# Kernel tuning notes

Measured on AMD Instinct MI355X. Metric: run time of the kernel, lower is better.

The kernel has to match this reference:

```python
import jax, jax.numpy as jnp
import numpy as np

N = 50000
E = 800000
DIM = 256
H = 8
D = DIM // H


def setup_inputs() -> dict:
    key = jax.random.key(0)
    ks = jax.random.split(key, 12)
    s = 1.0 / np.sqrt(DIM)
    return {
        "x": jax.random.normal(ks[0], (N, DIM), dtype=jnp.float32),
        "Wq": jax.random.normal(ks[1], (DIM, DIM), dtype=jnp.float32) * s,
        "bq": jax.random.normal(ks[2], (DIM,), dtype=jnp.float32) * 0.01,
        "Wk": jax.random.normal(ks[3], (DIM, DIM), dtype=jnp.float32) * s,
        "bk": jax.random.normal(ks[4], (DIM,), dtype=jnp.float32) * 0.01,
        "Wv": jax.random.normal(ks[5], (DIM, DIM), dtype=jnp.float32) * s,
        "bv": jax.random.normal(ks[6], (DIM,), dtype=jnp.float32) * 0.01,
        "Wo": jax.random.normal(ks[7], (DIM, DIM), dtype=jnp.float32) * s,
        "bo": jax.random.normal(ks[8], (DIM,), dtype=jnp.float32) * 0.01,
        "src": jax.random.randint(ks[9], (E,), 0, N, dtype=jnp.int32),
        "dst": jax.random.randint(ks[10], (E,), 0, N, dtype=jnp.int32),
    }


def reference(x, Wq, bq, Wk, bk, Wv, bv, Wo, bo, src, dst):
    # Linear projections (torch Linear: x @ W.T + b), then [N, H, D]
    q = (x @ Wq.T + bq).reshape(N, H, D)
    k = (x @ Wk.T + bk).reshape(N, H, D)
    v = (x @ Wv.T + bv).reshape(N, H, D)

    # u_dot_v: per-edge dot(queries[src], keys[dst]) -> [E, H]
    scores = jnp.einsum('ehd,ehd->eh', q[src], k[dst]) / jnp.sqrt(jnp.float32(D))

    # edge_softmax over incoming edges of each destination node
    smax = jax.ops.segment_max(scores, dst, num_segments=N)  # [N, H]
    e = jnp.exp(scores - smax[dst])                          # [E, H]
    ssum = jax.ops.segment_sum(e, dst, num_segments=N)       # [N, H]
    probs = e / ssum[dst]                                    # [E, H]

    # u_mul_e_sum: sum over incoming edges of values[src] * probs -> [N, H, D]
    out = jax.ops.segment_sum(v[src] * probs[:, :, None], dst, num_segments=N)

    out = out.reshape(N, DIM)
    return out @ Wo.T + bo  # dropout is identity at p=0 / eval
```

## Files before the change

### kernel.cpp

```cpp
#include <hip/hip_runtime.h>
#include <hip/hip_bf16.h>
#include <math.h>

#define DIMV 256
#define DV 32
#define QKVS 768

typedef __attribute__((ext_vector_type(8))) short bf16x8;
typedef __attribute__((ext_vector_type(4))) float f32x4;

#define EXPS(x) __expf(x)
#define SCORE_SCALE 0.17677669529663687f

static __device__ __forceinline__ unsigned short f2bf(float f) {
    unsigned x = __float_as_uint(f);
    x += 0x7FFF + ((x >> 16) & 1);
    return (unsigned short)(x >> 16);
}
static __device__ __forceinline__ float bf2f(unsigned short u) {
    return __uint_as_float(((unsigned)u) << 16);
}

static __device__ __forceinline__ void async16(const void* g, void* lds) {
    __builtin_amdgcn_global_load_lds(
        (const __attribute__((address_space(1))) void*)g,
        (__attribute__((address_space(3))) void*)lds, 16, 0, 0);
}


__global__ void cvt_w_count(const float* __restrict__ Wq, const float* __restrict__ Wk,
                            const float* __restrict__ Wv, const float* __restrict__ Wo,
                            unsigned short* __restrict__ Wcat,
                            const int* __restrict__ dst, int* __restrict__ deg, int E) {
    const float* W = blockIdx.y == 0 ? Wq : blockIdx.y == 1 ? Wk : blockIdx.y == 2 ? Wv : Wo;
    int i = blockIdx.x * 256 + threadIdx.x;
    float4 v = ((const float4*)W)[i];
    ushort4 o;
    o.x = f2bf(v.x); o.y = f2bf(v.y); o.z = f2bf(v.z); o.w = f2bf(v.w);
    ((ushort4*)(Wcat + (size_t)blockIdx.y * 65536))[i] = o;

    int gid = (blockIdx.y * gridDim.x + blockIdx.x) * 256 + threadIdx.x;
    int nthr = gridDim.x * gridDim.y * 256;
    for (int e = gid; e < E; e += nthr) atomicAdd(&deg[dst[e]], 1);
}


__global__ void zero_i32(int* __restrict__ p, int n) {
    int i = blockIdx.x * blockDim.x + threadIdx.x;
    if (i < n) p[i] = 0;
}

__global__ void block_sum(const int* __restrict__ deg, int* __restrict__ bsum, int n) {
    __shared__ int sm[256];
    int i = blockIdx.x * 256 + threadIdx.x;
    sm[threadIdx.x] = (i < n) ? deg[i] : 0;
    __syncthreads();
    for (int s = 128; s > 0; s >>= 1) {
        if (threadIdx.x < s) sm[threadIdx.x] += sm[threadIdx.x + s];
        __syncthreads();
    }
    if (threadIdx.x == 0) bsum[blockIdx.x] = sm[0];
}

__global__ void scan_bsum(int* __restrict__ bsum, int nb) {
    if (threadIdx.x == 0) {
        int r = 0;
        for (int i = 0; i < nb; ++i) { int v = bsum[i]; bsum[i] = r; r += v; }
    }
}

__global__ void scan_final(const int* __restrict__ deg, const int* __restrict__ bsum,
                           int* __restrict__ offsets, int* __restrict__ cursor, int n) {
    __shared__ int sm[256];
    int i = blockIdx.x * 256 + threadIdx.x;
    int v = (i < n) ? deg[i] : 0;
    sm[threadIdx.x] = v;
    __syncthreads();
    for (int s = 1; s < 256; s <<= 1) {
        int t = (threadIdx.x >= s) ? sm[threadIdx.x - s] : 0;
        __syncthreads();
        sm[threadIdx.x] += t;
        __syncthreads();
    }
    int excl = sm[threadIdx.x] - v + bsum[blockIdx.x];
    if (i < n) { offsets[i] = excl; cursor[i] = excl; }
    if (i == n - 1) offsets[n] = excl + v;
}


template<bool OF32, bool GUARD, int OSTRIDE, int MATSTRIDE>
static __device__ __forceinline__
void kloop(const bf16x8 (&a)[2][8], unsigned short (*Bls)[8192],
           const float* __restrict__ BiasLds, const unsigned short* __restrict__ Wcat,
           const unsigned* voff, void* __restrict__ Cout,
           int M, int ntiles, int row0, int rg, int cg, int lrow, int lkg, int w) {
    const int c = cg * 16 + lrow;
    for (int t = 0; t < ntiles; ++t) {
        if (GUARD) {
            __syncthreads();
        } else {
            asm volatile("s_waitcnt vmcnt(8)" ::: "memory");
            __builtin_amdgcn_s_barrier();
        }
        if (t + 1 < ntiles) {
            const char* gb = (const char*)Wcat + (size_t)(t + 1) * 16384;
            #pragma unroll
            for (int i = 0; i < 4; ++i)
                async16(gb + voff[i], (char*)&Bls[(t + 1) & 1][0] + (i * 4096 + w * 1024));
        }
        asm volatile("" ::: "memory");

        const unsigned short* bls = &Bls[t & 1][0];
        f32x4 acc0 = {0.f, 0.f, 0.f, 0.f};
        f32x4 acc1 = {0.f, 0.f, 0.f, 0.f};
        #pragma unroll
        for (int k0 = 0; k0 < 8; ++k0) {
            const bf16x8 bf = *(const bf16x8*)(bls + (size_t)(k0 * 128 + lkg * 32 + c) * 8);
            acc0 = __builtin_amdgcn_mfma_f32_16x16x32_bf16(a[0][k0], bf, acc0, 0, 0, 0);
            acc1 = __builtin_amdgcn_mfma_f32_16x16x32_bf16(a[1][k0], bf, acc1, 0, 0, 0);
        }

        int mat = t >> 3;
        int gcol = ((t & 7) << 5) + c;
        float bias = BiasLds[mat * 256 + gcol];
        unsigned cbase = (unsigned)mat * MATSTRIDE + gcol;
        #pragma unroll
        for (int mf = 0; mf < 2; ++mf) {
            f32x4 av = mf ? acc1 : acc0;
            #pragma unroll
            for (int r = 0; r < 4; ++r) {
                int row = row0 + rg * 32 + mf * 16 + lkg * 4 + r;
                if (!GUARD || row < M) {
                    float val = av[r] + bias;
                    if (OF32)
                        ((float*)Cout)[(size_t)row * OSTRIDE + cbase] = val;
                    else
                        ((unsigned short*)Cout)[(size_t)row * OSTRIDE + cbase] = f2bf(val);
                }
            }
        }
    }
}

template<bool AF32, bool OF32, int OSTRIDE, int MATSTRIDE, bool SCATTER>
__global__ __launch_bounds__(256, 4)
void gemm_fused(const void* __restrict__ Ain,
                const unsigned short* __restrict__ Wcat,
                const float* __restrict__ b0, const float* __restrict__ b1,
                const float* __restrict__ b2,
                void* __restrict__ Cout, int M, int ntiles, int scb,
                const int* __restrict__ esrc, const int* __restrict__ edst,
                int* __restrict__ cursor, int* __restrict__ perm_src, int E) {
    __shared__ unsigned short Bls[2][8192];
    __shared__ float BiasLds[768];

    if (SCATTER && (int)blockIdx.x < scb) {
        int nthr = scb * 256;
        for (int e = (int)blockIdx.x * 256 + (int)threadIdx.x; e < E; e += nthr)
            perm_src[atomicAdd(&cursor[edst[e]], 1)] = esrc[e];
        return;
    }
    const int bid = (int)blockIdx.x - (SCATTER ? scb : 0);
    const int tid = threadIdx.x;
    const int w = tid >> 6, lane = tid & 63;
    const int rg = w >> 1, cg = w & 1;
    const int lrow = lane & 15, lkg = lane >> 4;
    const int row0 = bid * 64;

    int nmat = ntiles >> 3;
    for (int i = tid; i < nmat * 256; i += 256) {
        const float* bp = (i >> 8) == 0 ? b0 : ((i >> 8) == 1 ? b1 : b2);
        BiasLds[i] = bp[i & 255];
    }

    unsigned voff[4];
    #pragma unroll
    for (int i = 0; i < 4; ++i) {
        unsigned idx = (unsigned)(i * 256 + w * 64 + lane);
        voff[i] = (idx & 31u) * 512u + (idx >> 7) * 64u + ((idx >> 5) & 3u) * 16u;
    }
    #pragma unroll
    for (int i = 0; i < 4; ++i)
        async16((const char*)Wcat + voff[i], (char*)&Bls[0][0] + (i * 4096 + w * 1024));

    bf16x8 a[2][8];
    #pragma unroll
    for (int m = 0; m < 2; ++m) {
        int row = row0 + rg * 32 + m * 16 + lrow;
        row = min(row, M - 1);
        if (AF32) {
            const float* ap = (const float*)Ain + (size_t)row * DIMV + lkg * 8;
            #pragma unroll
            for (int k0 = 0; k0 < 8; ++k0) {
                float4 f0 = *(const float4*)(ap + k0 * 32);
                float4 f1 = *(const float4*)(ap + k0 * 32 + 4);
                bf16x8 r;
                r[0] = (short)f2bf(f0.x); r[1] = (short)f2bf(f0.y);
                r[2] = (short)f2bf(f0.z); r[3] = (short)f2bf(f0.w);
                r[4] = (short)f2bf(f1.x); r[5] = (short)f2bf(f1.y);
                r[6] = (short)f2bf(f1.z); r[7] = (short)f2bf(f1.w);
                a[m][k0] = r;
            }
        } else {
            const unsigned short* ap = (const unsigned short*)Ain + (size_t)row * DIMV + lkg * 8;
            #pragma unroll
            for (int k0 = 0; k0 < 8; ++k0)
                a[m][k0] = *(const bf16x8*)(ap + k0 * 32);
        }
    }

    asm volatile("s_waitcnt vmcnt(0) lgkmcnt(0)" ::: "memory");
    __builtin_amdgcn_s_barrier();

    if (row0 + 64 <= M)
        kloop<OF32, false, OSTRIDE, MATSTRIDE>(a, Bls, BiasLds, Wcat, voff, Cout,
                                               M, ntiles, row0, rg, cg, lrow, lkg, w);
    else
        kloop<OF32, true, OSTRIDE, MATSTRIDE>(a, Bls, BiasLds, Wcat, voff, Cout,
                                              M, ntiles, row0, rg, cg, lrow, lkg, w);
}


__global__ __launch_bounds__(256)
void node_attn(const unsigned short* __restrict__ QKV,
               const int* __restrict__ offsets, const int* __restrict__ perm_src,
               unsigned short* __restrict__ attn, int N) {
    int wid = blockIdx.x * (blockDim.x >> 6) + (threadIdx.x >> 6);
    if (wid >= N) return;
    int lane = threadIdx.x & 63;
    unsigned col = (unsigned)((lane >> 3) * DV + (lane & 7) * 4);

    ushort4 kr = *(const ushort4*)(QKV + (size_t)wid * QKVS + 256 + col);
    float k0 = bf2f(kr.x) * SCORE_SCALE, k1 = bf2f(kr.y) * SCORE_SCALE;
    float k2 = bf2f(kr.z) * SCORE_SCALE, k3 = bf2f(kr.w) * SCORE_SCALE;

    float mA = -INFINITY, lA = 0.f, aA0 = 0.f, aA1 = 0.f, aA2 = 0.f, aA3 = 0.f;
    float mB = -INFINITY, lB = 0.f, aB0 = 0.f, aB1 = 0.f, aB2 = 0.f, aB3 = 0.f;

    auto upd = [&](ushort4 qr, ushort4 vr, float& m, float& l,
                   float& a0, float& a1, float& a2, float& a3) {
        float d = bf2f(qr.x) * k0 + bf2f(qr.y) * k1 + bf2f(qr.z) * k2 + bf2f(qr.w) * k3;
        d += __shfl_xor(d, 1); d += __shfl_xor(d, 2); d += __shfl_xor(d, 4);
        float mn = fmaxf(m, d);
        float sc = EXPS(m - mn);
        float pe = EXPS(d - mn);
        l = l * sc + pe;
        a0 = a0 * sc + pe * bf2f(vr.x);
        a1 = a1 * sc + pe * bf2f(vr.y);
        a2 = a2 * sc + pe * bf2f(vr.z);
        a3 = a3 * sc + pe * bf2f(vr.w);
        m = mn;
    };

    int e0 = offsets[wid], e1 = offsets[wid + 1];
    int rem = e1 - e0;
    int S = rem >> 1;
    int p = e0;

    if (S >= 1) {
        unsigned o0 = (unsigned)perm_src[p] * QKVS + col;
        unsigned o1 = (unsigned)perm_src[p + 1] * QKVS + col;
        ushort4 qA0 = *(const ushort4*)(QKV + o0);
        ushort4 vA0 = *(const ushort4*)(QKV + o0 + 512);
        ushort4 qA1 = *(const ushort4*)(QKV + o1);
        ushort4 vA1 = *(const ushort4*)(QKV + o1 + 512);
        unsigned n0 = 0, n1 = 0;
        if (S >= 2) {
            n0 = (unsigned)perm_src[p + 2] * QKVS + col;
            n1 = (unsigned)perm_src[p + 3] * QKVS + col;
        }
        ushort4 qB0, qB1, vB0, vB1;

        int s = 0;
        while (s + 2 <= S) {
            qB0 = *(const ushort4*)(QKV + n0);
            vB0 = *(const ushort4*)(QKV + n0 + 512);
            qB1 = *(const ushort4*)(QKV + n1);
            vB1 = *(const ushort4*)(QKV + n1 + 512);
            if (s + 2 < S) {
                n0 = (unsigned)perm_src[p + 2 * s + 4] * QKVS + col;
                n1 = (unsigned)perm_src[p + 2 * s + 5] * QKVS + col;
            }
            upd(qA0, vA0, mA, lA, aA0, aA1, aA2, aA3);
            upd(qA1, vA1, mB, lB, aB0, aB1, aB2, aB3);

            if (s + 2 < S) {
                qA0 = *(const ushort4*)(QKV + n0);
                vA0 = *(const ushort4*)(QKV + n0 + 512);
                qA1 = *(const ushort4*)(QKV + n1);
                vA1 = *(const ushort4*)(QKV + n1 + 512);
                if (s + 3 < S) {
                    n0 = (unsigned)perm_src[p + 2 * s + 6] * QKVS + col;
                    n1 = (unsigned)perm_src[p + 2 * s + 7] * QKVS + col;
                }
            }
            upd(qB0, vB0, mA, lA, aA0, aA1, aA2, aA3);
            upd(qB1, vB1, mB, lB, aB0, aB1, aB2, aB3);
            s += 2;
        }
        if (s < S) {
            upd(qA0, vA0, mA, lA, aA0, aA1, aA2, aA3);
            upd(qA1, vA1, mB, lB, aB0, aB1, aB2, aB3);
        }
    }
    if (rem & 1) {
        unsigned o0 = (unsigned)perm_src[e1 - 1] * QKVS + col;
        ushort4 q0 = *(const ushort4*)(QKV + o0);
        ushort4 v0 = *(const ushort4*)(QKV + o0 + 512);
        upd(q0, v0, mA, lA, aA0, aA1, aA2, aA3);
    }

    float mn = fmaxf(mA, mB);
    float scA = (lA > 0.f) ? EXPS(mA - mn) : 0.f;
    float scB = (lB > 0.f) ? EXPS(mB - mn) : 0.f;
    float l = lA * scA + lB * scB;
    float o0 = aA0 * scA + aB0 * scB;
    float o1 = aA1 * scA + aB1 * scB;
    float o2 = aA2 * scA + aB2 * scB;
    float o3 = aA3 * scA + aB3 * scB;
    float inv = (l > 0.f) ? 1.f / l : 0.f;

    ushort4 o;
    o.x = f2bf(o0 * inv); o.y = f2bf(o1 * inv); o.z = f2bf(o2 * inv); o.w = f2bf(o3 * inv);
    *(ushort4*)(attn + (size_t)wid * DIMV + col) = o;
}


extern "C" void kernel_launch(void* const* d_in, const int* in_sizes, int n_in,
                              void* d_out, int out_size, void* d_ws, size_t ws_size,
                              hipStream_t stream) {
    const float* x  = (const float*)d_in[0];
    const float* Wq = (const float*)d_in[1];
    const float* bq = (const float*)d_in[2];
    const float* Wk = (const float*)d_in[3];
    const float* bk = (const float*)d_in[4];
    const float* Wv = (const float*)d_in[5];
    const float* bv = (const float*)d_in[6];
    const float* Wo = (const float*)d_in[7];
    const float* bo = (const float*)d_in[8];
    const int* src  = (const int*)d_in[9];
    const int* dst  = (const int*)d_in[10];
    int N = in_sizes[0] / DIMV;
    int E = in_sizes[9];
    float* out = (float*)d_out;

    char* p = (char*)d_ws;
    auto alloc = [&](size_t bytes) {
        char* r = p;
        p += (bytes + 255) & ~(size_t)255;
        return r;
    };
    unsigned short* Wcat = (unsigned short*)alloc((size_t)4 * 65536 * 2);
    unsigned short* QKV  = (unsigned short*)alloc((size_t)N * QKVS * 2);
    unsigned short* attn = (unsigned short*)alloc((size_t)N * DIMV * 2);
    int* deg             = (int*)alloc((size_t)N * 4);
    int* offsets         = (int*)alloc((size_t)(N + 1) * 4);
    int* cursor          = (int*)alloc((size_t)N * 4);
    int* perm_src        = (int*)alloc((size_t)E * 4);
    int* bsum            = (int*)alloc((size_t)1024 * 4);

    int nb = (N + 255) / 256;
    zero_i32<<<nb, 256, 0, stream>>>(deg, N);
    dim3 gw(64, 4);
    cvt_w_count<<<gw, 256, 0, stream>>>(Wq, Wk, Wv, Wo, Wcat, dst, deg, E);

    block_sum<<<nb, 256, 0, stream>>>(deg, bsum, N);
    scan_bsum<<<1, 64, 0, stream>>>(bsum, nb);
    scan_final<<<nb, 256, 0, stream>>>(deg, bsum, offsets, cursor, N);

    int gemmBlocks = (N + 63) / 64;
    const int SCB = 160;
    gemm_fused<true, false, QKVS, 256, true><<<SCB + gemmBlocks, 256, 0, stream>>>(
        x, Wcat, bq, bk, bv, QKV, N, 24, SCB, src, dst, cursor, perm_src, E);

    node_attn<<<(N + 3) / 4, 256, 0, stream>>>(QKV, offsets, perm_src, attn, N);

    gemm_fused<false, true, DIMV, 0, false><<<gemmBlocks, 256, 0, stream>>>(
        attn, Wcat + (size_t)3 * 65536, bo, bo, bo, out, N, 8,
        0, nullptr, nullptr, nullptr, nullptr, 0);
}
```

Baseline: 284.4 us.

## Restructure projection GEMMs to 128-column register tiles with 4-stage weight pipeline

Replaces the per-32-column GEMM loop with a kernel where each wave owns 16 rows and accumulates a 16x128 output tile across the K dimension. Weight K-slices stream through a 4-deep LDS ring via async global-to-LDS loads, with explicit vmcnt waits. The bf16 QKV output is staged through LDS so each row is written as 16-byte vector stores. This raises register pressure (8 accumulators plus 8 B fragments) and drops the occupancy hint in exchange for more MFMA work per barrier and wider stores.

```diff
diff --git a/kernel.cpp b/kernel.cpp
--- a/kernel.cpp
+++ b/kernel.cpp
@@ -25,6 +25,14 @@
     __builtin_amdgcn_global_load_lds(
         (const __attribute__((address_space(1))) void*)g,
         (__attribute__((address_space(3))) void*)lds, 16, 0, 0);
+}
+
+static __device__ __forceinline__ void waitvm(int n) {
+    switch (n) {
+    case 0: asm volatile("s_waitcnt vmcnt(0)" ::: "memory"); break;
+    case 2: asm volatile("s_waitcnt vmcnt(2)" ::: "memory"); break;
+    default: asm volatile("s_waitcnt vmcnt(4)" ::: "memory"); break;
+    }
 }
 
 
@@ -88,136 +96,139 @@
 }
 
 
-template<bool OF32, bool GUARD, int OSTRIDE, int MATSTRIDE>
-static __device__ __forceinline__
-void kloop(const bf16x8 (&a)[2][8], unsigned short (*Bls)[8192],
-           const float* __restrict__ BiasLds, const unsigned short* __restrict__ Wcat,
-           const unsigned* voff, void* __restrict__ Cout,
-           int M, int ntiles, int row0, int rg, int cg, int lrow, int lkg, int w) {
-    const int c = cg * 16 + lrow;
-    for (int t = 0; t < ntiles; ++t) {
-        if (GUARD) {
-            __syncthreads();
-        } else {
-            asm volatile("s_waitcnt vmcnt(8)" ::: "memory");
-            __builtin_amdgcn_s_barrier();
-        }
-        if (t + 1 < ntiles) {
-            const char* gb = (const char*)Wcat + (size_t)(t + 1) * 16384;
-            #pragma unroll
-            for (int i = 0; i < 4; ++i)
-                async16(gb + voff[i], (char*)&Bls[(t + 1) & 1][0] + (i * 4096 + w * 1024));
-        }
-        asm volatile("" ::: "memory");
-
-        const unsigned short* bls = &Bls[t & 1][0];
-        f32x4 acc0 = {0.f, 0.f, 0.f, 0.f};
-        f32x4 acc1 = {0.f, 0.f, 0.f, 0.f};
-        #pragma unroll
-        for (int k0 = 0; k0 < 8; ++k0) {
-            const bf16x8 bf = *(const bf16x8*)(bls + (size_t)(k0 * 128 + lkg * 32 + c) * 8);
-            acc0 = __builtin_amdgcn_mfma_f32_16x16x32_bf16(a[0][k0], bf, acc0, 0, 0, 0);
-            acc1 = __builtin_amdgcn_mfma_f32_16x16x32_bf16(a[1][k0], bf, acc1, 0, 0, 0);
-        }
-
-        int mat = t >> 3;
-        int gcol = ((t & 7) << 5) + c;
-        float bias = BiasLds[mat * 256 + gcol];
-        unsigned cbase = (unsigned)mat * MATSTRIDE + gcol;
-        #pragma unroll
-        for (int mf = 0; mf < 2; ++mf) {
-            f32x4 av = mf ? acc1 : acc0;
-            #pragma unroll
-            for (int r = 0; r < 4; ++r) {
-                int row = row0 + rg * 32 + mf * 16 + lkg * 4 + r;
-                if (!GUARD || row < M) {
-                    float val = av[r] + bias;
-                    if (OF32)
-                        ((float*)Cout)[(size_t)row * OSTRIDE + cbase] = val;
-                    else
-                        ((unsigned short*)Cout)[(size_t)row * OSTRIDE + cbase] = f2bf(val);
-                }
-            }
-        }
-    }
-}
-
-template<bool AF32, bool OF32, int OSTRIDE, int MATSTRIDE, bool SCATTER>
-__global__ __launch_bounds__(256, 4)
-void gemm_fused(const void* __restrict__ Ain,
-                const unsigned short* __restrict__ Wcat,
-                const float* __restrict__ b0, const float* __restrict__ b1,
-                const float* __restrict__ b2,
-                void* __restrict__ Cout, int M, int ntiles, int scb,
-                const int* __restrict__ esrc, const int* __restrict__ edst,
-                int* __restrict__ cursor, int* __restrict__ perm_src, int E) {
-    __shared__ unsigned short Bls[2][8192];
-    __shared__ float BiasLds[768];
-
+template<bool AF32, bool OF32, int NCT, int OSTRIDE, bool SCATTER>
+__global__ __launch_bounds__(256)
+void gemm_reg(const void* __restrict__ Ain,
+              const unsigned short* __restrict__ Wb,
+              const float* __restrict__ b0, const float* __restrict__ b1,
+              const float* __restrict__ b2,
+              void* __restrict__ Cout, int M, int scb,
+              const int* __restrict__ esrc, const int* __restrict__ edst,
+              int* __restrict__ cursor, int* __restrict__ perm_src, int E) {
     if (SCATTER && (int)blockIdx.x < scb) {
         int nthr = scb * 256;
         for (int e = (int)blockIdx.x * 256 + (int)threadIdx.x; e < E; e += nthr)
             perm_src[atomicAdd(&cursor[edst[e]], 1)] = esrc[e];
         return;
     }
+    __shared__ unsigned short Bls[4][4096];
+    __shared__ unsigned short Tls[4 * 2176];
+    __shared__ float BiasLds[NCT * 128];
+
     const int bid = (int)blockIdx.x - (SCATTER ? scb : 0);
-    const int tid = threadIdx.x;
-    const int w = tid >> 6, lane = tid & 63;
-    const int rg = w >> 1, cg = w & 1;
+    const int tid = threadIdx.x, w = tid >> 6, lane = tid & 63;
     const int lrow = lane & 15, lkg = lane >> 4;
     const int row0 = bid * 64;
-
-    int nmat = ntiles >> 3;
-    for (int i = tid; i < nmat * 256; i += 256) {
-        const float* bp = (i >> 8) == 0 ? b0 : ((i >> 8) == 1 ? b1 : b2);
+    const int STOT = NCT * 8;
+
+    for (int i = tid; i < NCT * 128; i += 256) {
+        int mat = i >> 8;
+        const float* bp = mat == 0 ? b0 : (mat == 1 ? b1 : b2);
         BiasLds[i] = bp[i & 255];
     }
 
-    unsigned voff[4];
+    unsigned fb[2];
     #pragma unroll
-    for (int i = 0; i < 4; ++i) {
-        unsigned idx = (unsigned)(i * 256 + w * 64 + lane);
-        voff[i] = (idx & 31u) * 512u + (idx >> 7) * 64u + ((idx >> 5) & 3u) * 16u;
-    }
-    #pragma unroll
-    for (int i = 0; i < 4; ++i)
-        async16((const char*)Wcat + voff[i], (char*)&Bls[0][0] + (i * 4096 + w * 1024));
-
-    bf16x8 a[2][8];
-    #pragma unroll
-    for (int m = 0; m < 2; ++m) {
-        int row = row0 + rg * 32 + m * 16 + lrow;
-        row = min(row, M - 1);
+    for (int j = 0; j < 2; ++j) {
+        unsigned f = (unsigned)(w * 128 + j * 64 + lane);
+        fb[j] = (f >> 2) * 512u + (f & 3u) * 16u;
+    }
+    auto stage = [&](int s) {
+        unsigned base = ((unsigned)(s >> 3) << 16) + (unsigned)(s & 7) * 64u;
+        #pragma unroll
+        for (int j = 0; j < 2; ++j)
+            async16((const char*)Wb + base + fb[j],
+                    (char*)&Bls[s & 3][0] + (w * 2048 + j * 1024));
+    };
+    stage(0); stage(1); stage(2);
+
+    bf16x8 a[8];
+    {
+        int arow = min(row0 + w * 16 + lrow, M - 1);
         if (AF32) {
-            const float* ap = (const float*)Ain + (size_t)row * DIMV + lkg * 8;
-            #pragma unroll
-            for (int k0 = 0; k0 < 8; ++k0) {
-                float4 f0 = *(const float4*)(ap + k0 * 32);
-                float4 f1 = *(const float4*)(ap + k0 * 32 + 4);
+            const float* ap = (const float*)Ain + (size_t)arow * DIMV + lkg * 8;
+            #pragma unroll
+            for (int k = 0; k < 8; ++k) {
+                float4 f0 = *(const float4*)(ap + k * 32);
+                float4 f1 = *(const float4*)(ap + k * 32 + 4);
                 bf16x8 r;
                 r[0] = (short)f2bf(f0.x); r[1] = (short)f2bf(f0.y);
                 r[2] = (short)f2bf(f0.z); r[3] = (short)f2bf(f0.w);
                 r[4] = (short)f2bf(f1.x); r[5] = (short)f2bf(f1.y);
                 r[6] = (short)f2bf(f1.z); r[7] = (short)f2bf(f1.w);
-                a[m][k0] = r;
+                a[k] = r;
             }
         } else {
-            const unsigned short* ap = (const unsigned short*)Ain + (size_t)row * DIMV + lkg * 8;
-            #pragma unroll
-            for (int k0 = 0; k0 < 8; ++k0)
-                a[m][k0] = *(const bf16x8*)(ap + k0 * 32);
+            const unsigned short* ap = (const unsigned short*)Ain + (size_t)arow * DIMV + lkg * 8;
+            #pragma unroll
+            for (int k = 0; k < 8; ++k)
+                a[k] = *(const bf16x8*)(ap + k * 32);
         }
     }
 
     asm volatile("s_waitcnt vmcnt(0) lgkmcnt(0)" ::: "memory");
     __builtin_amdgcn_s_barrier();
 
-    if (row0 + 64 <= M)
-        kloop<OF32, false, OSTRIDE, MATSTRIDE>(a, Bls, BiasLds, Wcat, voff, Cout,
-                                               M, ntiles, row0, rg, cg, lrow, lkg, w);
-    else
-        kloop<OF32, true, OSTRIDE, MATSTRIDE>(a, Bls, BiasLds, Wcat, voff, Cout,
-                                              M, ntiles, row0, rg, cg, lrow, lkg, w);
+    #pragma unroll
+    for (int ct = 0; ct < NCT; ++ct) {
+        f32x4 acc[8] = {};
+        #pragma unroll
+        for (int k = 0; k < 8; ++k) {
+            const int s = ct * 8 + k;
+            if (s == STOT - 1)      waitvm(0);
+            else if (s == STOT - 2) waitvm(2);
+            else                    waitvm(4);
+            __builtin_amdgcn_s_barrier();
+            if (s + 3 < STOT) stage(s + 3);
+            asm volatile("" ::: "memory");
+
+            const char* base = (const char*)&Bls[s & 3][0];
+            bf16x8 bF[8];
+            #pragma unroll
+            for (int n = 0; n < 8; ++n)
+                bF[n] = *(const bf16x8*)(base + n * 1024 + lrow * 64 + lkg * 16);
+            asm volatile("s_waitcnt lgkmcnt(0)" ::: "memory");
+            __builtin_amdgcn_sched_barrier(0);
+            #pragma unroll
+            for (int n = 0; n < 8; ++n)
+                acc[n] = __builtin_amdgcn_mfma_f32_16x16x32_bf16(a[k], bF[n], acc[n], 0, 0, 0);
+        }
+        asm volatile("" ::: "memory");
+
+        if (OF32) {
+            #pragma unroll
+            for (int n = 0; n < 8; ++n) {
+                float bias = BiasLds[ct * 128 + n * 16 + lrow];
+                #pragma unroll
+                for (int r = 0; r < 4; ++r) {
+                    int grow = row0 + w * 16 + lkg * 4 + r;
+                    if (grow < M)
+                        ((float*)Cout)[(size_t)grow * OSTRIDE + ct * 128 + n * 16 + lrow] =
+                            acc[n][r] + bias;
+                }
+            }
+        } else {
+            #pragma unroll
+            for (int n = 0; n < 8; ++n) {
+                float bias = BiasLds[ct * 128 + n * 16 + lrow];
+                #pragma unroll
+                for (int r = 0; r < 4; ++r)
+                    Tls[w * 2176 + (lkg * 4 + r) * 136 + n * 16 + lrow] =
+                        f2bf(acc[n][r] + bias);
+            }
+            asm volatile("s_waitcnt lgkmcnt(0)" ::: "memory");
+            #pragma unroll
+            for (int j = 0; j < 4; ++j) {
+                int srow = j * 4 + lkg;
+                bf16x8 v = *(const bf16x8*)(&Tls[w * 2176 + srow * 136 + lrow * 8]);
+                int grow = row0 + w * 16 + srow;
+                if (grow < M)
+                    *(bf16x8*)((unsigned short*)Cout + (size_t)grow * OSTRIDE +
+                               ct * 128 + lrow * 8) = v;
+            }
+        }
+        asm volatile("" ::: "memory");
+    }
 }
 
 
@@ -361,6 +372,7 @@
 
     int nb = (N + 255) / 256;
     zero_i32<<<nb, 256, 0, stream>>>(deg, N);
+
     dim3 gw(64, 4);
     cvt_w_count<<<gw, 256, 0, stream>>>(Wq, Wk, Wv, Wo, Wcat, dst, deg, E);
 
@@ -368,14 +380,14 @@
     scan_bsum<<<1, 64, 0, stream>>>(bsum, nb);
     scan_final<<<nb, 256, 0, stream>>>(deg, bsum, offsets, cursor, N);
 
-    int gemmBlocks = (N + 63) / 64;
+    int rblocks = (N + 63) / 64;
     const int SCB = 160;
-    gemm_fused<true, false, QKVS, 256, true><<<SCB + gemmBlocks, 256, 0, stream>>>(
-        x, Wcat, bq, bk, bv, QKV, N, 24, SCB, src, dst, cursor, perm_src, E);
+    gemm_reg<true, false, 6, QKVS, true><<<SCB + rblocks, 256, 0, stream>>>(
+        x, Wcat, bq, bk, bv, QKV, N, SCB, src, dst, cursor, perm_src, E);
 
     node_attn<<<(N + 3) / 4, 256, 0, stream>>>(QKV, offsets, perm_src, attn, N);
 
-    gemm_fused<false, true, DIMV, 0, false><<<gemmBlocks, 256, 0, stream>>>(
-        attn, Wcat + (size_t)3 * 65536, bo, bo, bo, out, N, 8,
-        0, nullptr, nullptr, nullptr, nullptr, 0);
-}
+    gemm_reg<false, true, 2, DIMV, false><<<rblocks, 256, 0, stream>>>(
+        attn, Wcat + (size_t)3 * 65536, bo, bo, bo, out, N, 0,
+        nullptr, nullptr, nullptr, nullptr, 0);
+}
```

Result: faster. 277.8 us (-2.3%).
